# Performance work log

Hardware: AMD Instinct MI355X
Metric: run time of the kernel (lower is better)

## Reference

```python
import jax, jax.numpy as jnp
import numpy as np

B, F, W, H, D = 128, 1024, 32, 64, 64  # batch, n_features, window_size, hidden_state, output_dim


def setup_inputs() -> dict:
    key = jax.random.key(0)
    ks = jax.random.split(key, 8)
    sd = 0.05
    return {
        "x": jax.random.normal(ks[0], (B, F, W), jnp.float32),
        # dense_state: Dense(output_dim) on concat([cell, hidden]) -> [2H, D]
        "W_state": jax.random.normal(ks[1], (2 * H, D), jnp.float32) * sd,
        "b_state": jnp.zeros((D,), jnp.float32),
        # dense: Dense(output_dim, use_bias=False) on input last dim W -> [W, D]
        "W_in": jax.random.normal(ks[2], (W, D), jnp.float32) * sd,
        # Dense(1) scoring layer (shared; original re-creates it each call)
        "w_attn": jax.random.normal(ks[3], (D, 1), jnp.float32) * sd,
        "b_attn": jnp.zeros((1,), jnp.float32),
        # Keras LSTMCell params, gate order i, f, g(c~), o
        "Wx": jax.random.normal(ks[4], (F, 4 * H), jnp.float32) * sd,
        "Wh": jax.random.normal(ks[5], (H, 4 * H), jnp.float32) * sd,
        "b_lstm": jnp.zeros((4 * H,), jnp.float32),
    }


def _forward(x, W_state, b_state, W_in, w_attn, b_attn, Wx, Wh, b_lstm):
    b, f, w = x.shape
    h_dim = Wh.shape[0]
    # dense(input) is loop-invariant: [B, F, D]
    dense_in = jnp.einsum('bfw,wd->bfd', x, W_in)
    xs = jnp.moveaxis(x, 2, 0)  # [W, B, F]: per-timestep slices input[:, :, i]
    h0 = jnp.zeros((b, h_dim), x.dtype)
    c0 = jnp.zeros((b, h_dim), x.dtype)

    def step(carry, x_t):
        h, c = carry
        # original unpacks `s, h = state` with state=[h,c], so it concats [cell, hidden]
        attn_in = jnp.concatenate([c, h], axis=1)             # [B, 2H]
        z = jnp.tanh(attn_in @ W_state + b_state)[:, None, :] + dense_in  # [B, F, D]
        presoft = z @ w_attn + b_attn                         # [B, F, 1]
        # faithful: softmax over last (size-1) axis -> all ones
        alpha = jax.nn.softmax(presoft, axis=-1)
        x_tilde = alpha[..., 0] * x_t                         # [B, F]
        gates = x_tilde @ Wx + h @ Wh + b_lstm                # [B, 4H]
        i_g, f_g, g_g, o_g = jnp.split(gates, 4, axis=1)
        c_new = jax.nn.sigmoid(f_g) * c + jax.nn.sigmoid(i_g) * jnp.tanh(g_g)
        h_new = jax.nn.sigmoid(o_g) * jnp.tanh(c_new)
        # original appends state[1] == CELL state (due to the s,h swap)
        return (h_new, c_new), c_new

    _, outs = jax.lax.scan(step, (h0, c0), xs)                # [W, B, H]
    return jnp.transpose(outs, (1, 0, 2))                     # [B, W, H]


def reference(x, W_state, b_state, W_in, w_attn, b_attn, Wx, Wh, b_lstm):
    return _forward(x, W_state, b_state, W_in, w_attn, b_attn, Wx, Wh, b_lstm)
```

## Files before the change

### kernel.cpp

```cpp
#include <hip/hip_runtime.h>
#include <math.h>

#define B_   128
#define F_   1024
#define W_   32
#define H_   64
#define K4H  256
#define M_   (B_ * W_)
#define K2_  (2 * F_)

typedef __attribute__((ext_vector_type(8))) short  short8;
typedef __attribute__((ext_vector_type(4))) float  f32x4;

__device__ __forceinline__ unsigned bf16_rne(float v) {
  unsigned u = __float_as_uint(v);
  return (u + 0x7FFFu + ((u >> 16) & 1u)) >> 16;
}
__device__ __forceinline__ unsigned pack_hilo(float v) {
  unsigned hi = bf16_rne(v);
  float    hf = __uint_as_float(hi << 16);
  unsigned lo = bf16_rne(v - hf);
  return hi | (lo << 16);
}

__global__ __launch_bounds__(256) void conv_w(const float* __restrict__ Wx,
                                              unsigned* __restrict__ B2) {
  __shared__ unsigned T[256][17];
  const int tid = threadIdx.x;
  const int f0  = blockIdx.x * 16;
#pragma unroll
  for (int i = 0; i < 4; ++i) {
    int l = tid + i * 256;
    int n0 = (l & 63) * 4;
    int fl = l >> 6;
    float4 v = *(const float4*)&Wx[(size_t)(f0 + fl) * K4H + n0];
    T[n0 + 0][fl] = pack_hilo(v.x);
    T[n0 + 1][fl] = pack_hilo(v.y);
    T[n0 + 2][fl] = pack_hilo(v.z);
    T[n0 + 3][fl] = pack_hilo(v.w);
  }
  __syncthreads();
#pragma unroll
  for (int i = 0; i < 4; ++i) {
    int l  = tid + i * 256;
    int c4 = (l & 3) * 4;
    int n  = l >> 2;
    uint4 o;
    o.x = T[n][c4 + 0]; o.y = T[n][c4 + 1]; o.z = T[n][c4 + 2]; o.w = T[n][c4 + 3];
    *(uint4*)&B2[(size_t)n * (K2_ / 2) + f0 + c4] = o;
  }
}

template <int S>
__global__ __launch_bounds__(256, 2) void gemm_mfma(
    const float* __restrict__ x,
    const unsigned* __restrict__ B2,
    float* __restrict__ Gp) {
  constexpr int NIT = 32 / S;
  __shared__ unsigned lA[128 * 36];
  __shared__ unsigned lB[64 * 36];
  const int tid   = threadIdx.x;
  const int mtile = blockIdx.x;
  const int ntile = blockIdx.y;
  const int s     = blockIdx.z;
  const int wv = tid >> 6, lane = tid & 63;
  const int wm = wv & 1, wn = wv >> 1;
  const int lm = lane & 15, q = lane >> 4;

  f32x4 acc[4][2];
#pragma unroll
  for (int a = 0; a < 4; ++a)
#pragma unroll
    for (int bb = 0; bb < 2; ++bb) acc[a][bb] = (f32x4){0.f, 0.f, 0.f, 0.f};

  const int b0 = mtile * 4;
  float4 ax[4];
  uint4  bxr[2];

  auto prefetch = [&](int iter) {
    const int f0 = (s * NIT + iter) * 32;
#pragma unroll
    for (int i = 0; i < 4; ++i) {
      int l  = tid + i * 256;
      int t0 = (l & 7) * 4;
      int fl = (l >> 3) & 31;
      int bl = l >> 8;
      ax[i] = *(const float4*)&x[(((size_t)(b0 + bl)) * F_ + (f0 + fl)) * W_ + t0];
    }
#pragma unroll
    for (int i = 0; i < 2; ++i) {
      int l   = tid + i * 256;
      int c16 = l & 7;
      int nl  = l >> 3;
      bxr[i] = *(const uint4*)&B2[(size_t)(ntile * 64 + nl) * (K2_ / 2) + f0 + c16 * 4];
    }
  };

  prefetch(0);
  for (int iter = 0; iter < NIT; ++iter) {
    __syncthreads();
#pragma unroll
    for (int i = 0; i < 4; ++i) {
      int l  = tid + i * 256;
      int t0 = (l & 7) * 4;
      int fl = (l >> 3) & 31;
      int bl = l >> 8;
      int m  = bl * 32 + t0;
      lA[(m + 0) * 36 + fl] = pack_hilo(ax[i].x);
      lA[(m + 1) * 36 + fl] = pack_hilo(ax[i].y);
      lA[(m + 2) * 36 + fl] = pack_hilo(ax[i].z);
      lA[(m + 3) * 36 + fl] = pack_hilo(ax[i].w);
    }
#pragma unroll
    for (int i = 0; i < 2; ++i) {
      int l   = tid + i * 256;
      int c16 = l & 7;
      int nl  = l >> 3;
      *(uint4*)&lB[nl * 36 + c16 * 4] = bxr[i];
    }
    __syncthreads();
    if (iter + 1 < NIT) prefetch(iter + 1);
#pragma unroll
    for (int step = 0; step < 2; ++step) {
      short8 aF[4], bF[2];
#pragma unroll
      for (int mt = 0; mt < 4; ++mt) {
        int row = wm * 64 + mt * 16 + lm;
        aF[mt] = *(const short8*)&lA[row * 36 + step * 16 + q * 4];
      }
#pragma unroll
      for (int nt = 0; nt < 2; ++nt) {
        int row = wn * 32 + nt * 16 + lm;
        bF[nt] = *(const short8*)&lB[row * 36 + step * 16 + q * 4];
      }
#pragma unroll
      for (int mt = 0; mt < 4; ++mt)
#pragma unroll
        for (int nt = 0; nt < 2; ++nt)
          acc[mt][nt] = __builtin_amdgcn_mfma_f32_16x16x32_bf16(
              aF[mt], bF[nt], acc[mt][nt], 0, 0, 0);
    }
  }
  float* Gs = Gp + (size_t)s * ((size_t)M_ * K4H);
#pragma unroll
  for (int mt = 0; mt < 4; ++mt)
#pragma unroll
    for (int nt = 0; nt < 2; ++nt)
#pragma unroll
      for (int r = 0; r < 4; ++r) {
        int m = mtile * 128 + wm * 64 + mt * 16 + q * 4 + r;
        int n = ntile * 64 + wn * 32 + nt * 16 + lm;
        Gs[(size_t)m * K4H + n] = acc[mt][nt][r];
      }
}

__device__ __forceinline__ float bcastlane(float v, int l) {
  return __uint_as_float(__builtin_amdgcn_readlane(__float_as_uint(v), l));
}
__device__ __forceinline__ float sigm(float v)   { return 1.f / (1.f + __expf(-v)); }
__device__ __forceinline__ float tanh_f(float v) { return 1.f - 2.f / (__expf(2.f * v) + 1.f); }

template <int S>
__global__ __launch_bounds__(64, 1) void lstm_seq(
    const float* __restrict__ Gp, const float* __restrict__ Wh,
    const float* __restrict__ bl, float* __restrict__ out) {
  const int b = blockIdx.x, u = threadIdx.x;

  float wI[64], wF[64], wG[64], wO[64];
#pragma unroll
  for (int j = 0; j < 64; ++j) {
    const float* r = Wh + j * K4H;
    wI[j] = r[u];
    wF[j] = r[u + 64];
    wG[j] = r[u + 128];
    wO[j] = r[u + 192];
  }
  const float bI = bl[u], bF = bl[u + 64], bG = bl[u + 128], bO = bl[u + 192];
  const size_t base = (size_t)b * W_ * K4H;
  const size_t sstr = (size_t)M_ * K4H;

  float h = 0.f, c = 0.f;
  float pI = 0.f, pF = 0.f, pG = 0.f, pO = 0.f;
#pragma unroll
  for (int ss = 0; ss < S; ++ss) {
    const float* g0 = Gp + ss * sstr + base;
    pI += g0[u]; pF += g0[u + 64]; pG += g0[u + 128]; pO += g0[u + 192];
  }
  for (int t = 0; t < W_; ++t) {
    float nI = 0.f, nF = 0.f, nG = 0.f, nO = 0.f;
    if (t + 1 < W_) {
#pragma unroll
      for (int ss = 0; ss < S; ++ss) {
        const float* gn = Gp + ss * sstr + base + (size_t)(t + 1) * K4H;
        nI += gn[u]; nF += gn[u + 64]; nG += gn[u + 128]; nO += gn[u + 192];
      }
    }
    float aI = pI + bI, aF2 = pF + bF, aG = pG + bG, aO = pO + bO;
#pragma unroll
    for (int j = 0; j < 64; ++j) {
      float hj = bcastlane(h, j);
      aI  = fmaf(hj, wI[j], aI);
      aF2 = fmaf(hj, wF[j], aF2);
      aG  = fmaf(hj, wG[j], aG);
      aO  = fmaf(hj, wO[j], aO);
    }
    float si = sigm(aI), sf = sigm(aF2), tg = tanh_f(aG), so = sigm(aO);
    c = fmaf(sf, c, si * tg);
    h = so * tanh_f(c);
    out[((size_t)b * W_ + t) * H_ + u] = c;
    pI = nI; pF = nF; pG = nG; pO = nO;
  }
}

extern "C" void kernel_launch(void* const* d_in, const int* in_sizes, int n_in,
                              void* d_out, int out_size, void* d_ws, size_t ws_size,
                              hipStream_t stream) {
  const float* x      = (const float*)d_in[0];
  const float* Wx     = (const float*)d_in[6];
  const float* Wh     = (const float*)d_in[7];
  const float* b_lstm = (const float*)d_in[8];
  float* out = (float*)d_out;

  const size_t gbytes = (size_t)M_ * K4H * sizeof(float);

  if (ws_size >= 2 * gbytes + (1u << 20)) {
    float*    Gp = (float*)d_ws;
    unsigned* B2 = (unsigned*)((char*)d_ws + 2 * gbytes);
    conv_w      <<<dim3(64),       dim3(256), 0, stream>>>(Wx, B2);
    gemm_mfma<2><<<dim3(32, 4, 2), dim3(256), 0, stream>>>(x, B2, Gp);
    lstm_seq<2> <<<dim3(B_),       dim3(64),  0, stream>>>(Gp, Wh, b_lstm, out);
  } else {
    float*    Gp = (float*)d_ws;
    unsigned* B2 = (unsigned*)((char*)d_ws + gbytes);
    conv_w      <<<dim3(64),       dim3(256), 0, stream>>>(Wx, B2);
    gemm_mfma<1><<<dim3(32, 4, 1), dim3(256), 0, stream>>>(x, B2, Gp);
    lstm_seq<1> <<<dim3(B_),       dim3(64),  0, stream>>>(Gp, Wh, b_lstm, out);
  }
}
```

Before: 143.4 us.

## Widen GEMM N-tile, split-K by four, and spread LSTM gates across four waves

```diff
diff --git a/kernel.cpp b/kernel.cpp
--- a/kernel.cpp
+++ b/kernel.cpp
@@ -52,13 +52,13 @@
 }
 
 template <int S>
-__global__ __launch_bounds__(256, 2) void gemm_mfma(
+__global__ __launch_bounds__(256, 1) void gemm_mfma(
     const float* __restrict__ x,
     const unsigned* __restrict__ B2,
     float* __restrict__ Gp) {
   constexpr int NIT = 32 / S;
   __shared__ unsigned lA[128 * 36];
-  __shared__ unsigned lB[64 * 36];
+  __shared__ unsigned lB[128 * 36];
   const int tid   = threadIdx.x;
   const int mtile = blockIdx.x;
   const int ntile = blockIdx.y;
@@ -67,15 +67,15 @@
   const int wm = wv & 1, wn = wv >> 1;
   const int lm = lane & 15, q = lane >> 4;
 
-  f32x4 acc[4][2];
+  f32x4 acc[4][4];
 #pragma unroll
   for (int a = 0; a < 4; ++a)
 #pragma unroll
-    for (int bb = 0; bb < 2; ++bb) acc[a][bb] = (f32x4){0.f, 0.f, 0.f, 0.f};
+    for (int bb = 0; bb < 4; ++bb) acc[a][bb] = (f32x4){0.f, 0.f, 0.f, 0.f};
 
   const int b0 = mtile * 4;
   float4 ax[4];
-  uint4  bxr[2];
+  uint4  bxr[4];
 
   auto prefetch = [&](int iter) {
     const int f0 = (s * NIT + iter) * 32;
@@ -88,15 +88,16 @@
       ax[i] = *(const float4*)&x[(((size_t)(b0 + bl)) * F_ + (f0 + fl)) * W_ + t0];
     }
 #pragma unroll
-    for (int i = 0; i < 2; ++i) {
+    for (int i = 0; i < 4; ++i) {
       int l   = tid + i * 256;
       int c16 = l & 7;
       int nl  = l >> 3;
-      bxr[i] = *(const uint4*)&B2[(size_t)(ntile * 64 + nl) * (K2_ / 2) + f0 + c16 * 4];
+      bxr[i] = *(const uint4*)&B2[(size_t)(ntile * 128 + nl) * (K2_ / 2) + f0 + c16 * 4];
     }
   };
 
   prefetch(0);
+  const int jx = (tid >> 3) & 3;
   for (int iter = 0; iter < NIT; ++iter) {
     __syncthreads();
 #pragma unroll
@@ -105,14 +106,16 @@
       int t0 = (l & 7) * 4;
       int fl = (l >> 3) & 31;
       int bl = l >> 8;
-      int m  = bl * 32 + t0;
-      lA[(m + 0) * 36 + fl] = pack_hilo(ax[i].x);
-      lA[(m + 1) * 36 + fl] = pack_hilo(ax[i].y);
-      lA[(m + 2) * 36 + fl] = pack_hilo(ax[i].z);
-      lA[(m + 3) * 36 + fl] = pack_hilo(ax[i].w);
-    }
-#pragma unroll
-    for (int i = 0; i < 2; ++i) {
+      int m0 = bl * 32 + t0;
+      float vals[4] = {ax[i].x, ax[i].y, ax[i].z, ax[i].w};
+#pragma unroll
+      for (int j = 0; j < 4; ++j) {
+        int jj = j ^ jx;
+        lA[(m0 + jj) * 36 + fl] = pack_hilo(vals[jj]);
+      }
+    }
+#pragma unroll
+    for (int i = 0; i < 4; ++i) {
       int l   = tid + i * 256;
       int c16 = l & 7;
       int nl  = l >> 3;
@@ -122,21 +125,21 @@
     if (iter + 1 < NIT) prefetch(iter + 1);
 #pragma unroll
     for (int step = 0; step < 2; ++step) {
-      short8 aF[4], bF[2];
+      short8 aF[4], bF[4];
 #pragma unroll
       for (int mt = 0; mt < 4; ++mt) {
         int row = wm * 64 + mt * 16 + lm;
         aF[mt] = *(const short8*)&lA[row * 36 + step * 16 + q * 4];
       }
 #pragma unroll
-      for (int nt = 0; nt < 2; ++nt) {
-        int row = wn * 32 + nt * 16 + lm;
+      for (int nt = 0; nt < 4; ++nt) {
+        int row = wn * 64 + nt * 16 + lm;
         bF[nt] = *(const short8*)&lB[row * 36 + step * 16 + q * 4];
       }
 #pragma unroll
       for (int mt = 0; mt < 4; ++mt)
 #pragma unroll
-        for (int nt = 0; nt < 2; ++nt)
+        for (int nt = 0; nt < 4; ++nt)
           acc[mt][nt] = __builtin_amdgcn_mfma_f32_16x16x32_bf16(
               aF[mt], bF[nt], acc[mt][nt], 0, 0, 0);
     }
@@ -145,11 +148,11 @@
 #pragma unroll
   for (int mt = 0; mt < 4; ++mt)
 #pragma unroll
-    for (int nt = 0; nt < 2; ++nt)
+    for (int nt = 0; nt < 4; ++nt)
 #pragma unroll
       for (int r = 0; r < 4; ++r) {
         int m = mtile * 128 + wm * 64 + mt * 16 + q * 4 + r;
-        int n = ntile * 64 + wn * 32 + nt * 16 + lm;
+        int n = ntile * 128 + wn * 64 + nt * 16 + lm;
         Gs[(size_t)m * K4H + n] = acc[mt][nt][r];
       }
 }
@@ -161,54 +164,53 @@
 __device__ __forceinline__ float tanh_f(float v) { return 1.f - 2.f / (__expf(2.f * v) + 1.f); }
 
 template <int S>
-__global__ __launch_bounds__(64, 1) void lstm_seq(
+__global__ __launch_bounds__(256, 1) void lstm_seq(
     const float* __restrict__ Gp, const float* __restrict__ Wh,
     const float* __restrict__ bl, float* __restrict__ out) {
-  const int b = blockIdx.x, u = threadIdx.x;
-
-  float wI[64], wF[64], wG[64], wO[64];
-#pragma unroll
-  for (int j = 0; j < 64; ++j) {
-    const float* r = Wh + j * K4H;
-    wI[j] = r[u];
-    wF[j] = r[u + 64];
-    wG[j] = r[u + 128];
-    wO[j] = r[u + 192];
-  }
-  const float bI = bl[u], bF = bl[u + 64], bG = bl[u + 128], bO = bl[u + 192];
-  const size_t base = (size_t)b * W_ * K4H;
+  __shared__ float sact[2][4][64];
+  const int b = blockIdx.x, tid = threadIdx.x;
+  const int w = tid >> 6, u = tid & 63;
+  const int k = w * 64 + u;
+
+  float wc[64];
+#pragma unroll
+  for (int j = 0; j < 64; ++j) wc[j] = Wh[j * K4H + k];
+  const float bk = bl[k];
+  const size_t base = (size_t)b * W_ * K4H + k;
   const size_t sstr = (size_t)M_ * K4H;
 
   float h = 0.f, c = 0.f;
-  float pI = 0.f, pF = 0.f, pG = 0.f, pO = 0.f;
-#pragma unroll
-  for (int ss = 0; ss < S; ++ss) {
-    const float* g0 = Gp + ss * sstr + base;
-    pI += g0[u]; pF += g0[u + 64]; pG += g0[u + 128]; pO += g0[u + 192];
-  }
+  float p = 0.f;
+#pragma unroll
+  for (int ss = 0; ss < S; ++ss) p += Gp[ss * sstr + base];
+
   for (int t = 0; t < W_; ++t) {
-    float nI = 0.f, nF = 0.f, nG = 0.f, nO = 0.f;
+    float nx = 0.f;
     if (t + 1 < W_) {
 #pragma unroll
-      for (int ss = 0; ss < S; ++ss) {
-        const float* gn = Gp + ss * sstr + base + (size_t)(t + 1) * K4H;
-        nI += gn[u]; nF += gn[u + 64]; nG += gn[u + 128]; nO += gn[u + 192];
-      }
-    }
-    float aI = pI + bI, aF2 = pF + bF, aG = pG + bG, aO = pO + bO;
-#pragma unroll
-    for (int j = 0; j < 64; ++j) {
-      float hj = bcastlane(h, j);
-      aI  = fmaf(hj, wI[j], aI);
-      aF2 = fmaf(hj, wF[j], aF2);
-      aG  = fmaf(hj, wG[j], aG);
-      aO  = fmaf(hj, wO[j], aO);
-    }
-    float si = sigm(aI), sf = sigm(aF2), tg = tanh_f(aG), so = sigm(aO);
+      for (int ss = 0; ss < S; ++ss)
+        nx += Gp[ss * sstr + base + (size_t)(t + 1) * K4H];
+    }
+    float a0 = p + bk, a1 = 0.f, a2 = 0.f, a3 = 0.f;
+#pragma unroll
+    for (int j = 0; j < 64; j += 4) {
+      a0 = fmaf(bcastlane(h, j),     wc[j],     a0);
+      a1 = fmaf(bcastlane(h, j + 1), wc[j + 1], a1);
+      a2 = fmaf(bcastlane(h, j + 2), wc[j + 2], a2);
+      a3 = fmaf(bcastlane(h, j + 3), wc[j + 3], a3);
+    }
+    float g = (a0 + a1) + (a2 + a3);
+    float act = (w == 2) ? tanh_f(g) : sigm(g);
+    sact[t & 1][w][u] = act;
+    __syncthreads();
+    float si = sact[t & 1][0][u];
+    float sf = sact[t & 1][1][u];
+    float tg = sact[t & 1][2][u];
+    float so = sact[t & 1][3][u];
     c = fmaf(sf, c, si * tg);
     h = so * tanh_f(c);
-    out[((size_t)b * W_ + t) * H_ + u] = c;
-    pI = nI; pF = nF; pG = nG; pO = nO;
+    if (w == 0) out[((size_t)b * W_ + t) * H_ + u] = c;
+    p = nx;
   }
 }
 
@@ -223,17 +225,23 @@
 
   const size_t gbytes = (size_t)M_ * K4H * sizeof(float);
 
-  if (ws_size >= 2 * gbytes + (1u << 20)) {
+  if (ws_size >= 4 * gbytes + (1u << 20)) {
+    float*    Gp = (float*)d_ws;
+    unsigned* B2 = (unsigned*)((char*)d_ws + 4 * gbytes);
+    conv_w      <<<dim3(64),       dim3(256), 0, stream>>>(Wx, B2);
+    gemm_mfma<4><<<dim3(32, 2, 4), dim3(256), 0, stream>>>(x, B2, Gp);
+    lstm_seq<4> <<<dim3(B_),       dim3(256), 0, stream>>>(Gp, Wh, b_lstm, out);
+  } else if (ws_size >= 2 * gbytes + (1u << 20)) {
     float*    Gp = (float*)d_ws;
     unsigned* B2 = (unsigned*)((char*)d_ws + 2 * gbytes);
     conv_w      <<<dim3(64),       dim3(256), 0, stream>>>(Wx, B2);
-    gemm_mfma<2><<<dim3(32, 4, 2), dim3(256), 0, stream>>>(x, B2, Gp);
-    lstm_seq<2> <<<dim3(B_),       dim3(64),  0, stream>>>(Gp, Wh, b_lstm, out);
+    gemm_mfma<2><<<dim3(32, 2, 2), dim3(256), 0, stream>>>(x, B2, Gp);
+    lstm_seq<2> <<<dim3(B_),       dim3(256), 0, stream>>>(Gp, Wh, b_lstm, out);
   } else {
     float*    Gp = (float*)d_ws;
     unsigned* B2 = (unsigned*)((char*)d_ws + gbytes);
     conv_w      <<<dim3(64),       dim3(256), 0, stream>>>(Wx, B2);
-    gemm_mfma<1><<<dim3(32, 4, 1), dim3(256), 0, stream>>>(x, B2, Gp);
-    lstm_seq<1> <<<dim3(B_),       dim3(64),  0, stream>>>(Gp, Wh, b_lstm, out);
-  }
-}
+    gemm_mfma<1><<<dim3(32, 2, 1), dim3(256), 0, stream>>>(x, B2, Gp);
+    lstm_seq<1> <<<dim3(B_),       dim3(256), 0, stream>>>(Gp, Wh, b_lstm, out);
+  }
+}
```

New measurement: 121.3 us. -15.5%, faster.
